# Kernel tuning notes

Measured on AMD Instinct MI355X. Metric: run time of the kernel, lower is better.

Reference implementation:

```python
import jax, jax.numpy as jnp
import numpy as np

N, E, D = 50000, 1600000, 64


def setup_inputs() -> dict:
    key = jax.random.key(0)
    ks = jax.random.split(key, 10)
    s = 1.0 / np.sqrt(D)
    return {
        "x": jax.random.normal(ks[0], (N, D), dtype=jnp.float32),
        "edge_index": jax.random.randint(ks[1], (2, E), 0, N, dtype=jnp.int64),
        "edge_weight": jax.random.uniform(ks[2], (E,), dtype=jnp.float32),
        "W_rel1": jax.random.uniform(ks[3], (D, D), jnp.float32, -s, s),
        "b_rel1": jax.random.uniform(ks[4], (D,), jnp.float32, -s, s),
        "W_root1": jax.random.uniform(ks[5], (D, D), jnp.float32, -s, s),
        "W_rel2": jax.random.uniform(ks[6], (D, D), jnp.float32, -s, s),
        "b_rel2": jax.random.uniform(ks[7], (D,), jnp.float32, -s, s),
        "W_root2": jax.random.uniform(ks[8], (D, D), jnp.float32, -s, s),
    }


def graph_conv(x, src, dst, edge_weight, W_rel, b_rel, W_root):
    # message: edge_weight * x[src]; aggregate: sum into dst
    msg = edge_weight[:, None] * x[src]                      # [E, D]
    agg = jax.ops.segment_sum(msg, dst, num_segments=x.shape[0])  # [N, D]
    return agg @ W_rel.T + b_rel + x @ W_root.T


def reference(x, edge_index, edge_weight, W_rel1, b_rel1, W_root1, W_rel2, b_rel2, W_root2):
    src, dst = edge_index[0], edge_index[1]
    h = jax.nn.relu(graph_conv(x, src, dst, edge_weight, W_rel1, b_rel1, W_root1))
    # dropout is identity in eval mode
    h = jax.nn.relu(graph_conv(h, src, dst, edge_weight, W_rel2, b_rel2, W_root2))
    return h
```

## Files before the change

kernel.cpp:

```cpp
#include <hip/hip_runtime.h>


#define NN 50000
#define DD 64
#define EE 1600000
#define NPB 64
#define NB  ((NN + NPB - 1) / NPB)
#define PAD 2560
#define CHUNK 8192
#define NC ((EE + CHUNK - 1) / CHUNK)

static_assert(NC <= 256, "colscan_kernel scan width must cover all chunks");
static_assert(NB <= 1024, "LDS cursor arrays sized for NB");

typedef __attribute__((ext_vector_type(8))) short short8;
typedef __attribute__((ext_vector_type(4))) float f32x4;

__device__ __forceinline__ unsigned short f2bf(float f) {
    unsigned u = __float_as_uint(f);
    u += 0x7FFF + ((u >> 16) & 1);
    return (unsigned short)(u >> 16);
}
__device__ __forceinline__ float bflo(unsigned u) {
    return __uint_as_float(u << 16);
}
__device__ __forceinline__ float bfhi(unsigned u) {
    return __uint_as_float(u & 0xFFFF0000u);
}
__device__ __forceinline__ unsigned char f2fp8(float f) {
    unsigned p = __builtin_amdgcn_cvt_pk_fp8_f32(f, f, 0, false);
    return (unsigned char)(p & 0xFF);
}

#define XS_STR 72
#define WS_STR 72

template <typename TIn>
__device__ __forceinline__ void transform_body(
    int blk, int t,
    const TIn* __restrict__ xin,
    const float* __restrict__ Wrel, const float* __restrict__ Wroot,
    const float* __restrict__ bias,
    unsigned char* __restrict__ Z8, unsigned short* __restrict__ Yb,
    unsigned short* Xs, unsigned short* Ws)
{
    const int node0 = blk * 64;

#pragma unroll
    for (int i = 0; i < 8; ++i) {
        int flat = i * 256 + t;
        int row  = flat >> 4;
        int c4   = flat & 15;
        const float* src = (row < 64 ? Wrel + row * 64
                                     : Wroot + (row - 64) * 64) + c4 * 4;
        float4 v = *(const float4*)src;
        unsigned short* d = &Ws[row * WS_STR + c4 * 4];
        d[0] = f2bf(v.x); d[1] = f2bf(v.y); d[2] = f2bf(v.z); d[3] = f2bf(v.w);
    }
    if constexpr (sizeof(TIn) == 4) {
#pragma unroll
        for (int i = 0; i < 4; ++i) {
            int flat = i * 256 + t;
            int row  = flat >> 4;
            int c4   = flat & 15;
            int node = node0 + row;
            float4 v = make_float4(0.f, 0.f, 0.f, 0.f);
            if (node < NN) v = *(const float4*)((const float*)xin + (size_t)node * 64 + c4 * 4);
            unsigned short* d = &Xs[row * XS_STR + c4 * 4];
            d[0] = f2bf(v.x); d[1] = f2bf(v.y); d[2] = f2bf(v.z); d[3] = f2bf(v.w);
        }
    } else {
#pragma unroll
        for (int i = 0; i < 2; ++i) {
            int flat = i * 256 + t;
            int row  = flat >> 3;
            int c8   = flat & 7;
            int node = node0 + row;
            short8 v = {0,0,0,0,0,0,0,0};
            if (node < NN)
                v = *(const short8*)((const unsigned short*)xin + (size_t)node * 64 + c8 * 8);
            *(short8*)&Xs[row * XS_STR + c8 * 8] = v;
        }
    }
    __syncthreads();

    const int w    = t >> 6;
    const int lane = t & 63;
    const int l15  = lane & 15;
    const int quad = lane >> 4;

    short8 a0 = *(const short8*)&Xs[(w * 16 + l15) * XS_STR + quad * 8];
    short8 a1 = *(const short8*)&Xs[(w * 16 + l15) * XS_STR + 32 + quad * 8];

#pragma unroll
    for (int f = 0; f < 8; ++f) {
        short8 b0 = *(const short8*)&Ws[(f * 16 + l15) * WS_STR + quad * 8];
        short8 b1 = *(const short8*)&Ws[(f * 16 + l15) * WS_STR + 32 + quad * 8];
        f32x4 acc = {0.f, 0.f, 0.f, 0.f};
        acc = __builtin_amdgcn_mfma_f32_16x16x32_bf16(a0, b0, acc, 0, 0, 0);
        acc = __builtin_amdgcn_mfma_f32_16x16x32_bf16(a1, b1, acc, 0, 0, 0);
        const int col = f * 16 + l15;
#pragma unroll
        for (int r = 0; r < 4; ++r) {
            int node = node0 + w * 16 + quad * 4 + r;
            if (node < NN) {
                if (col < 64) Z8[(size_t)node * 64 + col] = f2fp8(acc[r]);
                else          Yb[(size_t)node * 64 + (col - 64)] =
                                  f2bf(acc[r] + bias[col - 64]);
            }
        }
    }
}

__global__ __launch_bounds__(256) void hist_t1_kernel(
    const int* __restrict__ ei, int* __restrict__ hist,
    const float* __restrict__ x,
    const float* __restrict__ Wrel, const float* __restrict__ Wroot,
    const float* __restrict__ bias,
    unsigned char* __restrict__ Z8, unsigned short* __restrict__ Yb)
{
    __shared__ int lh[NB];
    __shared__ unsigned short Xs[64 * XS_STR];
    __shared__ unsigned short Ws[128 * WS_STR];
    const int t = threadIdx.x;

    if (blockIdx.x < NC) {
        const int c = blockIdx.x;
        for (int b = t; b < NB; b += 256) lh[b] = 0;
        __syncthreads();
        const int base = c * CHUNK;
#pragma unroll 4
        for (int i = 0; i < CHUNK; i += 256) {
            int e = base + i + t;
            if (e < EE) atomicAdd(&lh[ei[EE + e] >> 6], 1);
        }
        __syncthreads();
        for (int b = t; b < NB; b += 256) hist[c * NB + b] = lh[b];
    } else {
        transform_body<float>(blockIdx.x - NC, t, x, Wrel, Wroot, bias,
                              Z8, Yb, Xs, Ws);
    }
}

__global__ __launch_bounds__(256) void transform2_kernel(
    const unsigned short* __restrict__ xin,
    const float* __restrict__ Wrel, const float* __restrict__ Wroot,
    const float* __restrict__ bias,
    unsigned char* __restrict__ Z8, unsigned short* __restrict__ Yb)
{
    __shared__ unsigned short Xs[64 * XS_STR];
    __shared__ unsigned short Ws[128 * WS_STR];
    transform_body<unsigned short>(blockIdx.x, threadIdx.x, xin, Wrel, Wroot,
                                   bias, Z8, Yb, Xs, Ws);
}

__global__ __launch_bounds__(256) void colscan_kernel(
    const int* __restrict__ hist, int* __restrict__ offs, int* __restrict__ bsz)
{
    __shared__ int part[256];
    const int b = blockIdx.x, t = threadIdx.x;
    int h = (t < NC) ? hist[t * NB + b] : 0;
    part[t] = h;
    __syncthreads();
    for (int off = 1; off < 256; off <<= 1) {
        int v = (t >= off) ? part[t - off] : 0;
        __syncthreads();
        part[t] += v;
        __syncthreads();
    }
    if (t < NC) offs[t * NB + b] = b * PAD + (part[t] - h);
    if (t == 255) bsz[b] = part[255];
}

__global__ __launch_bounds__(256) void bin_kernel(
    const int* __restrict__ ei, const float* __restrict__ ew,
    const int* __restrict__ offs, unsigned* __restrict__ epk)
{
    __shared__ int cur[NB];
    const int c = blockIdx.x, t = threadIdx.x;
    for (int b = t; b < NB; b += 256) cur[b] = offs[c * NB + b];
    __syncthreads();
    const int base = c * CHUNK;
    for (int i = 0; i < CHUNK; i += 256) {
        int e = base + i + t;
        if (e < EE) {
            int src = ei[e];
            int dst = ei[EE + e];
            unsigned q = (unsigned)fmaf(ew[e], 1023.0f, 0.5f);
            int pos = atomicAdd(&cur[dst >> 6], 1);
            epk[pos] = (unsigned)src | ((unsigned)(dst & 63) << 16) | (q << 22);
        }
    }
}

__global__ __launch_bounds__(512) void aggregate_sort_kernel(
    const unsigned* __restrict__ Z1,
    const uint2* __restrict__ Y4,
    const int* __restrict__ bsz,
    unsigned* __restrict__ epk,
    int* __restrict__ beg, int* __restrict__ endo,
    void* __restrict__ Hout)
{
    __shared__ int      cnt[NPB];
    __shared__ int      nbeg[NPB];
    __shared__ int      cur[NPB];
    __shared__ unsigned stage[PAD];
    const int bk = blockIdx.x, t = threadIdx.x;
    const int base = bk * PAD;
    int sz = bsz[bk];
    if (sz > PAD) sz = PAD;

    if (t < NPB) cnt[t] = 0;
    __syncthreads();
    for (int i = t; i < sz; i += 512)
        atomicAdd(&cnt[(epk[base + i] >> 16) & 63], 1);
    __syncthreads();

    if (t < 64) {
        int c = cnt[t];
        int v = c;
        for (int off = 1; off < 64; off <<= 1) {
            int u = __shfl_up(v, off);
            if (t >= off) v += u;
        }
        int ex = v - c;
        nbeg[t] = ex;
        cur[t]  = ex;
        int g = bk * NPB + t;
        if (g < NN) { beg[g] = base + ex; endo[g] = base + ex + c; }
    }
    __syncthreads();

    for (int i = t; i < sz; i += 512) {
        unsigned p = epk[base + i];
        int pos = atomicAdd(&cur[(p >> 16) & 63], 1);
        float w = (float)(p >> 22) * (1.0f / 1023.0f);
        stage[pos] = (p & 0xFFFFu) | ((unsigned)f2bf(w) << 16);
    }
    __syncthreads();

    for (int i = t; i < sz; i += 512)
        epk[base + i] = stage[i];

    const int lane = t & 63;
    const int wv   = t >> 6;
    const int s = lane & 15;
    const int q = lane >> 4;

#pragma unroll
    for (int k = 0; k < 8; ++k) {
        const int n6   = wv * 8 + k;
        const int node = bk * 64 + n6;
        const int b = nbeg[n6];
        const int e = b + cnt[n6];

        float a0 = 0.f, a1 = 0.f, a2 = 0.f, a3 = 0.f;
        int i = b;
        for (; i + 16 <= e; i += 16) {
            unsigned pA = stage[i + q];
            unsigned pB = stage[i + 4 + q];
            unsigned pC = stage[i + 8 + q];
            unsigned pD = stage[i + 12 + q];
            unsigned zA = Z1[(pA & 0xFFFF) * 16 + s];
            unsigned zB = Z1[(pB & 0xFFFF) * 16 + s];
            unsigned zC = Z1[(pC & 0xFFFF) * 16 + s];
            unsigned zD = Z1[(pD & 0xFFFF) * 16 + s];
            float wA = __uint_as_float(pA & 0xFFFF0000u);
            float wB = __uint_as_float(pB & 0xFFFF0000u);
            float wC = __uint_as_float(pC & 0xFFFF0000u);
            float wD = __uint_as_float(pD & 0xFFFF0000u);
            a0 = fmaf(wA, __builtin_amdgcn_cvt_f32_fp8(zA, 0), a0);
            a1 = fmaf(wA, __builtin_amdgcn_cvt_f32_fp8(zA, 1), a1);
            a2 = fmaf(wA, __builtin_amdgcn_cvt_f32_fp8(zA, 2), a2);
            a3 = fmaf(wA, __builtin_amdgcn_cvt_f32_fp8(zA, 3), a3);
            a0 = fmaf(wB, __builtin_amdgcn_cvt_f32_fp8(zB, 0), a0);
            a1 = fmaf(wB, __builtin_amdgcn_cvt_f32_fp8(zB, 1), a1);
            a2 = fmaf(wB, __builtin_amdgcn_cvt_f32_fp8(zB, 2), a2);
            a3 = fmaf(wB, __builtin_amdgcn_cvt_f32_fp8(zB, 3), a3);
            a0 = fmaf(wC, __builtin_amdgcn_cvt_f32_fp8(zC, 0), a0);
            a1 = fmaf(wC, __builtin_amdgcn_cvt_f32_fp8(zC, 1), a1);
            a2 = fmaf(wC, __builtin_amdgcn_cvt_f32_fp8(zC, 2), a2);
            a3 = fmaf(wC, __builtin_amdgcn_cvt_f32_fp8(zC, 3), a3);
            a0 = fmaf(wD, __builtin_amdgcn_cvt_f32_fp8(zD, 0), a0);
            a1 = fmaf(wD, __builtin_amdgcn_cvt_f32_fp8(zD, 1), a1);
            a2 = fmaf(wD, __builtin_amdgcn_cvt_f32_fp8(zD, 2), a2);
            a3 = fmaf(wD, __builtin_amdgcn_cvt_f32_fp8(zD, 3), a3);
        }
        for (; i < e; i += 4) {
            int ee = i + q;
            unsigned p = (ee < e) ? stage[ee] : 0u;
            unsigned z = Z1[(p & 0xFFFF) * 16 + s];
            float w = __uint_as_float(p & 0xFFFF0000u);
            a0 = fmaf(w, __builtin_amdgcn_cvt_f32_fp8(z, 0), a0);
            a1 = fmaf(w, __builtin_amdgcn_cvt_f32_fp8(z, 1), a1);
            a2 = fmaf(w, __builtin_amdgcn_cvt_f32_fp8(z, 2), a2);
            a3 = fmaf(w, __builtin_amdgcn_cvt_f32_fp8(z, 3), a3);
        }

        a0 += __shfl_xor(a0, 16); a0 += __shfl_xor(a0, 32);
        a1 += __shfl_xor(a1, 16); a1 += __shfl_xor(a1, 32);
        a2 += __shfl_xor(a2, 16); a2 += __shfl_xor(a2, 32);
        a3 += __shfl_xor(a3, 16); a3 += __shfl_xor(a3, 32);

        if (q == 0 && node < NN) {
            const uint2 y4 = Y4[node * 16 + s];
            float r0 = fmaxf(a0 + bflo(y4.x), 0.0f);
            float r1 = fmaxf(a1 + bfhi(y4.x), 0.0f);
            float r2 = fmaxf(a2 + bflo(y4.y), 0.0f);
            float r3 = fmaxf(a3 + bfhi(y4.y), 0.0f);
            uint2 o;
            o.x = (unsigned)f2bf(r0) | ((unsigned)f2bf(r1) << 16);
            o.y = (unsigned)f2bf(r2) | ((unsigned)f2bf(r3) << 16);
            ((uint2*)Hout)[node * 16 + s] = o;
        }
    }
}

__global__ __launch_bounds__(256) void aggregate2_kernel(
    const unsigned* __restrict__ Z1,
    const uint2* __restrict__ Y4,
    const int* __restrict__ beg, const int* __restrict__ endo,
    const unsigned* __restrict__ epk, float4* __restrict__ Hout)
{
    const int lane = threadIdx.x & 63;
    const int node = blockIdx.x * 4 + (threadIdx.x >> 6);
    if (node >= NN) return;
    const int s = lane & 15;
    const int q = lane >> 4;

    const int b = beg[node];
    const int e = endo[node];
    const uint2 y4 = Y4[node * 16 + s];

    float a0 = 0.f, a1 = 0.f, a2 = 0.f, a3 = 0.f;
    int i = b;
    for (; i + 16 <= e; i += 16) {
        unsigned pA = epk[i + q];
        unsigned pB = epk[i + 4 + q];
        unsigned pC = epk[i + 8 + q];
        unsigned pD = epk[i + 12 + q];
        unsigned zA = Z1[(pA & 0xFFFF) * 16 + s];
        unsigned zB = Z1[(pB & 0xFFFF) * 16 + s];
        unsigned zC = Z1[(pC & 0xFFFF) * 16 + s];
        unsigned zD = Z1[(pD & 0xFFFF) * 16 + s];
        float wA = __uint_as_float(pA & 0xFFFF0000u);
        float wB = __uint_as_float(pB & 0xFFFF0000u);
        float wC = __uint_as_float(pC & 0xFFFF0000u);
        float wD = __uint_as_float(pD & 0xFFFF0000u);
        a0 = fmaf(wA, __builtin_amdgcn_cvt_f32_fp8(zA, 0), a0);
        a1 = fmaf(wA, __builtin_amdgcn_cvt_f32_fp8(zA, 1), a1);
        a2 = fmaf(wA, __builtin_amdgcn_cvt_f32_fp8(zA, 2), a2);
        a3 = fmaf(wA, __builtin_amdgcn_cvt_f32_fp8(zA, 3), a3);
        a0 = fmaf(wB, __builtin_amdgcn_cvt_f32_fp8(zB, 0), a0);
        a1 = fmaf(wB, __builtin_amdgcn_cvt_f32_fp8(zB, 1), a1);
        a2 = fmaf(wB, __builtin_amdgcn_cvt_f32_fp8(zB, 2), a2);
        a3 = fmaf(wB, __builtin_amdgcn_cvt_f32_fp8(zB, 3), a3);
        a0 = fmaf(wC, __builtin_amdgcn_cvt_f32_fp8(zC, 0), a0);
        a1 = fmaf(wC, __builtin_amdgcn_cvt_f32_fp8(zC, 1), a1);
        a2 = fmaf(wC, __builtin_amdgcn_cvt_f32_fp8(zC, 2), a2);
        a3 = fmaf(wC, __builtin_amdgcn_cvt_f32_fp8(zC, 3), a3);
        a0 = fmaf(wD, __builtin_amdgcn_cvt_f32_fp8(zD, 0), a0);
        a1 = fmaf(wD, __builtin_amdgcn_cvt_f32_fp8(zD, 1), a1);
        a2 = fmaf(wD, __builtin_amdgcn_cvt_f32_fp8(zD, 2), a2);
        a3 = fmaf(wD, __builtin_amdgcn_cvt_f32_fp8(zD, 3), a3);
    }
    for (; i < e; i += 4) {
        int ee = i + q;
        unsigned p = (ee < e) ? epk[ee] : 0u;
        unsigned z = Z1[(p & 0xFFFF) * 16 + s];
        float w = __uint_as_float(p & 0xFFFF0000u);
        a0 = fmaf(w, __builtin_amdgcn_cvt_f32_fp8(z, 0), a0);
        a1 = fmaf(w, __builtin_amdgcn_cvt_f32_fp8(z, 1), a1);
        a2 = fmaf(w, __builtin_amdgcn_cvt_f32_fp8(z, 2), a2);
        a3 = fmaf(w, __builtin_amdgcn_cvt_f32_fp8(z, 3), a3);
    }

    a0 += __shfl_xor(a0, 16); a0 += __shfl_xor(a0, 32);
    a1 += __shfl_xor(a1, 16); a1 += __shfl_xor(a1, 32);
    a2 += __shfl_xor(a2, 16); a2 += __shfl_xor(a2, 32);
    a3 += __shfl_xor(a3, 16); a3 += __shfl_xor(a3, 32);

    if (q == 0) {
        float r0 = fmaxf(a0 + bflo(y4.x), 0.0f);
        float r1 = fmaxf(a1 + bfhi(y4.x), 0.0f);
        float r2 = fmaxf(a2 + bflo(y4.y), 0.0f);
        float r3 = fmaxf(a3 + bfhi(y4.y), 0.0f);
        Hout[node * 16 + s] = make_float4(r0, r1, r2, r3);
    }
}

extern "C" void kernel_launch(void* const* d_in, const int* in_sizes, int n_in,
                              void* d_out, int out_size, void* d_ws, size_t ws_size,
                              hipStream_t stream)
{
    const float* x     = (const float*)d_in[0];
    const int*   ei    = (const int*)  d_in[1];
    const float* ew    = (const float*)d_in[2];
    const float* Wrel1 = (const float*)d_in[3];
    const float* brel1 = (const float*)d_in[4];
    const float* Wroot1= (const float*)d_in[5];
    const float* Wrel2 = (const float*)d_in[6];
    const float* brel2 = (const float*)d_in[7];
    const float* Wroot2= (const float*)d_in[8];

    float* out = (float*)d_out;

    const size_t ND = (size_t)NN * DD;
    char* w = (char*)d_ws;
    unsigned char*  Z8 = (unsigned char*)w;
    unsigned short* Yb = (unsigned short*)(w + ND);
    unsigned short* Hb = (unsigned short*)(w + ND * 3);
    unsigned* epk = (unsigned*)(w + ND * 5);
    int* bsz  = (int*)(w + ND * 5 + (size_t)NB * PAD * 4);
    int* hist = bsz + NB;
    int* offs = hist + (size_t)NC * NB;
    int* beg  = offs + (size_t)NC * NB;
    int* endo = beg + NN;

    const int tb = (NN + 63) / 64;
    const int ab = (NN + 3) / 4;

    hist_t1_kernel<<<NC + tb, 256, 0, stream>>>(ei, hist, x, Wrel1, Wroot1,
                                                brel1, Z8, Yb);
    colscan_kernel<<<NB, 256, 0, stream>>>(hist, offs, bsz);
    bin_kernel    <<<NC, 256, 0, stream>>>(ei, ew, offs, epk);

    aggregate_sort_kernel<<<NB, 512, 0, stream>>>(
        (const unsigned*)Z8, (const uint2*)Yb, bsz, epk, beg, endo, Hb);

    transform2_kernel<<<tb, 256, 0, stream>>>(Hb, Wrel2, Wroot2, brel2, Z8, Yb);
    aggregate2_kernel<<<ab, 256, 0, stream>>>(
        (const unsigned*)Z8, (const uint2*)Yb, beg, endo, epk, (float4*)out);
}
```

Before: 195.6 us.

## Fuse layer-2 transform into sort-aggregate kernel and pre-convert W2 to bf16

Layer-1 aggregation now writes its ReLU output into shared memory, and the same block immediately runs the layer-2 MFMA transform on it. This removes the separate transform2 launch and the global round-trip of the intermediate bf16 activations. The layer-2 weights are converted to bf16 once, in extra blocks of the colscan kernel, so each block does not convert them again. Costs: more LDS per aggregate block, which may lower occupancy, and separate Z8b/Yb2 buffers so layer-1's Z8/Yb are not overwritten while other blocks still read them.

```diff
diff --git a/kernel.cpp b/kernel.cpp
--- a/kernel.cpp
+++ b/kernel.cpp
@@ -35,10 +35,9 @@
 #define XS_STR 72
 #define WS_STR 72
 
-template <typename TIn>
-__device__ __forceinline__ void transform_body(
+__device__ __forceinline__ void transform_body_f32(
     int blk, int t,
-    const TIn* __restrict__ xin,
+    const float* __restrict__ xin,
     const float* __restrict__ Wrel, const float* __restrict__ Wroot,
     const float* __restrict__ bias,
     unsigned char* __restrict__ Z8, unsigned short* __restrict__ Yb,
@@ -57,30 +56,16 @@
         unsigned short* d = &Ws[row * WS_STR + c4 * 4];
         d[0] = f2bf(v.x); d[1] = f2bf(v.y); d[2] = f2bf(v.z); d[3] = f2bf(v.w);
     }
-    if constexpr (sizeof(TIn) == 4) {
-#pragma unroll
-        for (int i = 0; i < 4; ++i) {
-            int flat = i * 256 + t;
-            int row  = flat >> 4;
-            int c4   = flat & 15;
-            int node = node0 + row;
-            float4 v = make_float4(0.f, 0.f, 0.f, 0.f);
-            if (node < NN) v = *(const float4*)((const float*)xin + (size_t)node * 64 + c4 * 4);
-            unsigned short* d = &Xs[row * XS_STR + c4 * 4];
-            d[0] = f2bf(v.x); d[1] = f2bf(v.y); d[2] = f2bf(v.z); d[3] = f2bf(v.w);
-        }
-    } else {
-#pragma unroll
-        for (int i = 0; i < 2; ++i) {
-            int flat = i * 256 + t;
-            int row  = flat >> 3;
-            int c8   = flat & 7;
-            int node = node0 + row;
-            short8 v = {0,0,0,0,0,0,0,0};
-            if (node < NN)
-                v = *(const short8*)((const unsigned short*)xin + (size_t)node * 64 + c8 * 8);
-            *(short8*)&Xs[row * XS_STR + c8 * 8] = v;
-        }
+#pragma unroll
+    for (int i = 0; i < 4; ++i) {
+        int flat = i * 256 + t;
+        int row  = flat >> 4;
+        int c4   = flat & 15;
+        int node = node0 + row;
+        float4 v = make_float4(0.f, 0.f, 0.f, 0.f);
+        if (node < NN) v = *(const float4*)(xin + (size_t)node * 64 + c4 * 4);
+        unsigned short* d = &Xs[row * XS_STR + c4 * 4];
+        d[0] = f2bf(v.x); d[1] = f2bf(v.y); d[2] = f2bf(v.z); d[3] = f2bf(v.w);
     }
     __syncthreads();
 
@@ -137,28 +122,34 @@
         __syncthreads();
         for (int b = t; b < NB; b += 256) hist[c * NB + b] = lh[b];
     } else {
-        transform_body<float>(blockIdx.x - NC, t, x, Wrel, Wroot, bias,
-                              Z8, Yb, Xs, Ws);
-    }
-}
-
-__global__ __launch_bounds__(256) void transform2_kernel(
-    const unsigned short* __restrict__ xin,
-    const float* __restrict__ Wrel, const float* __restrict__ Wroot,
-    const float* __restrict__ bias,
-    unsigned char* __restrict__ Z8, unsigned short* __restrict__ Yb)
-{
-    __shared__ unsigned short Xs[64 * XS_STR];
-    __shared__ unsigned short Ws[128 * WS_STR];
-    transform_body<unsigned short>(blockIdx.x, threadIdx.x, xin, Wrel, Wroot,
-                                   bias, Z8, Yb, Xs, Ws);
-}
-
-__global__ __launch_bounds__(256) void colscan_kernel(
-    const int* __restrict__ hist, int* __restrict__ offs, int* __restrict__ bsz)
-{
+        transform_body_f32(blockIdx.x - NC, t, x, Wrel, Wroot, bias,
+                           Z8, Yb, Xs, Ws);
+    }
+}
+
+__global__ __launch_bounds__(256) void colscan_wconv_kernel(
+    const int* __restrict__ hist, int* __restrict__ offs, int* __restrict__ bsz,
+    const float* __restrict__ Wrel2, const float* __restrict__ Wroot2,
+    unsigned short* __restrict__ Wb2)
+{
+    const int t = threadIdx.x;
+    if (blockIdx.x >= NB) {
+        const int b2 = blockIdx.x - NB;
+#pragma unroll
+        for (int i = 0; i < 4; ++i) {
+            int flat = b2 * 1024 + i * 256 + t;
+            int row  = flat >> 4;
+            int c4   = flat & 15;
+            const float* src = (row < 64 ? Wrel2 + row * 64
+                                         : Wroot2 + (row - 64) * 64) + c4 * 4;
+            float4 v = *(const float4*)src;
+            unsigned short* d = &Wb2[row * 64 + c4 * 4];
+            d[0] = f2bf(v.x); d[1] = f2bf(v.y); d[2] = f2bf(v.z); d[3] = f2bf(v.w);
+        }
+        return;
+    }
     __shared__ int part[256];
-    const int b = blockIdx.x, t = threadIdx.x;
+    const int b = blockIdx.x;
     int h = (t < NC) ? hist[t * NB + b] : 0;
     part[t] = h;
     __syncthreads();
@@ -193,22 +184,35 @@
     }
 }
 
-__global__ __launch_bounds__(512) void aggregate_sort_kernel(
+__global__ __launch_bounds__(512) void aggsort_t2_kernel(
     const unsigned* __restrict__ Z1,
     const uint2* __restrict__ Y4,
     const int* __restrict__ bsz,
     unsigned* __restrict__ epk,
     int* __restrict__ beg, int* __restrict__ endo,
-    void* __restrict__ Hout)
+    const unsigned short* __restrict__ Wb2,
+    const float* __restrict__ bias2,
+    unsigned char* __restrict__ Z8b, unsigned short* __restrict__ Yb2)
 {
     __shared__ int      cnt[NPB];
     __shared__ int      nbeg[NPB];
     __shared__ int      cur[NPB];
     __shared__ unsigned stage[PAD];
+    __shared__ unsigned short Xs[64 * XS_STR];
+    __shared__ unsigned short Ws[128 * WS_STR];
     const int bk = blockIdx.x, t = threadIdx.x;
     const int base = bk * PAD;
     int sz = bsz[bk];
     if (sz > PAD) sz = PAD;
+
+#pragma unroll
+    for (int i = 0; i < 2; ++i) {
+        int flat = i * 512 + t;
+        int row  = flat >> 3;
+        int c8   = flat & 7;
+        *(short8*)&Ws[row * WS_STR + c8 * 8] =
+            *(const short8*)&Wb2[row * 64 + c8 * 8];
+    }
 
     if (t < NPB) cnt[t] = 0;
     __syncthreads();
@@ -253,6 +257,7 @@
         const int node = bk * 64 + n6;
         const int b = nbeg[n6];
         const int e = b + cnt[n6];
+        const uint2 y4 = (node < NN) ? Y4[node * 16 + s] : make_uint2(0u, 0u);
 
         float a0 = 0.f, a1 = 0.f, a2 = 0.f, a3 = 0.f;
         int i = b;
@@ -302,8 +307,7 @@
         a2 += __shfl_xor(a2, 16); a2 += __shfl_xor(a2, 32);
         a3 += __shfl_xor(a3, 16); a3 += __shfl_xor(a3, 32);
 
-        if (q == 0 && node < NN) {
-            const uint2 y4 = Y4[node * 16 + s];
+        if (q == 0) {
             float r0 = fmaxf(a0 + bflo(y4.x), 0.0f);
             float r1 = fmaxf(a1 + bfhi(y4.x), 0.0f);
             float r2 = fmaxf(a2 + bflo(y4.y), 0.0f);
@@ -311,7 +315,35 @@
             uint2 o;
             o.x = (unsigned)f2bf(r0) | ((unsigned)f2bf(r1) << 16);
             o.y = (unsigned)f2bf(r2) | ((unsigned)f2bf(r3) << 16);
-            ((uint2*)Hout)[node * 16 + s] = o;
+            *(uint2*)&Xs[n6 * XS_STR + s * 4] = o;
+        }
+    }
+    __syncthreads();
+
+    {
+        const int w4  = wv & 3;
+        const int fh  = (wv >> 2) * 4;
+        const int l15 = lane & 15;
+        const int quad = lane >> 4;
+        short8 A0 = *(const short8*)&Xs[(w4 * 16 + l15) * XS_STR + quad * 8];
+        short8 A1 = *(const short8*)&Xs[(w4 * 16 + l15) * XS_STR + 32 + quad * 8];
+#pragma unroll
+        for (int f = fh; f < fh + 4; ++f) {
+            short8 B0 = *(const short8*)&Ws[(f * 16 + l15) * WS_STR + quad * 8];
+            short8 B1 = *(const short8*)&Ws[(f * 16 + l15) * WS_STR + 32 + quad * 8];
+            f32x4 acc = {0.f, 0.f, 0.f, 0.f};
+            acc = __builtin_amdgcn_mfma_f32_16x16x32_bf16(A0, B0, acc, 0, 0, 0);
+            acc = __builtin_amdgcn_mfma_f32_16x16x32_bf16(A1, B1, acc, 0, 0, 0);
+            const int col = f * 16 + l15;
+#pragma unroll
+            for (int r = 0; r < 4; ++r) {
+                int node = bk * 64 + w4 * 16 + quad * 4 + r;
+                if (node < NN) {
+                    if (col < 64) Z8b[(size_t)node * 64 + col] = f2fp8(acc[r]);
+                    else          Yb2[(size_t)node * 64 + (col - 64)] =
+                                      f2bf(acc[r] + bias2[col - 64]);
+                }
+            }
         }
     }
 }
@@ -407,11 +439,13 @@
 
     const size_t ND = (size_t)NN * DD;
     char* w = (char*)d_ws;
-    unsigned char*  Z8 = (unsigned char*)w;
-    unsigned short* Yb = (unsigned short*)(w + ND);
-    unsigned short* Hb = (unsigned short*)(w + ND * 3);
-    unsigned* epk = (unsigned*)(w + ND * 5);
-    int* bsz  = (int*)(w + ND * 5 + (size_t)NB * PAD * 4);
+    unsigned char*  Z8  = (unsigned char*)w;
+    unsigned short* Yb  = (unsigned short*)(w + ND);
+    unsigned char*  Z8b = (unsigned char*)(w + ND * 3);
+    unsigned short* Yb2 = (unsigned short*)(w + ND * 4);
+    unsigned* epk = (unsigned*)(w + ND * 6);
+    unsigned short* Wb2 = (unsigned short*)(w + ND * 6 + (size_t)NB * PAD * 4);
+    int* bsz  = (int*)(Wb2 + 128 * 64);
     int* hist = bsz + NB;
     int* offs = hist + (size_t)NC * NB;
     int* beg  = offs + (size_t)NC * NB;
@@ -422,13 +456,14 @@
 
     hist_t1_kernel<<<NC + tb, 256, 0, stream>>>(ei, hist, x, Wrel1, Wroot1,
                                                 brel1, Z8, Yb);
-    colscan_kernel<<<NB, 256, 0, stream>>>(hist, offs, bsz);
-    bin_kernel    <<<NC, 256, 0, stream>>>(ei, ew, offs, epk);
-
-    aggregate_sort_kernel<<<NB, 512, 0, stream>>>(
-        (const unsigned*)Z8, (const uint2*)Yb, bsz, epk, beg, endo, Hb);
-
-    transform2_kernel<<<tb, 256, 0, stream>>>(Hb, Wrel2, Wroot2, brel2, Z8, Yb);
+    colscan_wconv_kernel<<<NB + 2, 256, 0, stream>>>(hist, offs, bsz,
+                                                     Wrel2, Wroot2, Wb2);
+    bin_kernel<<<NC, 256, 0, stream>>>(ei, ew, offs, epk);
+
+    aggsort_t2_kernel<<<NB, 512, 0, stream>>>(
+        (const unsigned*)Z8, (const uint2*)Yb, bsz, epk, beg, endo,
+        Wb2, brel2, Z8b, Yb2);
+
     aggregate2_kernel<<<ab, 256, 0, stream>>>(
-        (const unsigned*)Z8, (const uint2*)Yb, beg, endo, epk, (float4*)out);
-}
+        (const unsigned*)Z8b, (const uint2*)Yb2, beg, endo, epk, (float4*)out);
+}
```

Result: faster. 185.9 us (-5.0%).
